# Kernel tuning notes

Measured on AMD Instinct MI355X. Metric: run time of the kernel, lower is better.

Reference implementation:

```python
import jax, jax.numpy as jnp
import numpy as np

B, L, H, C = 1, 512, 1024, 2


def setup_inputs() -> dict:
    key = jax.random.key(0)
    k1, k2, k3 = jax.random.split(key, 3)
    lm_output = jax.random.normal(k1, (B, L, H), dtype=jnp.float32)
    # torch Linear weight layout: [out_features, in_features]
    W1 = jax.random.normal(k2, (H, 2 * H), dtype=jnp.float32) * 0.02
    b1 = jnp.zeros((H,), dtype=jnp.float32)
    W2 = jax.random.normal(k3, (C, H), dtype=jnp.float32) * 0.02
    b2 = jnp.zeros((C,), dtype=jnp.float32)
    return {"lm_output": lm_output, "W1": W1, "b1": b1, "W2": W2, "b2": b2}


def reference(lm_output, W1, b1, W2, b2):
    # pair_emb[b,i,j] = concat(lm_output[b,j], lm_output[b,i])
    # Linear(concat(a,b)) decomposes: split W1 into the halves acting on each part.
    Wa = W1[:, :H]  # acts on lm_output_a (the j / column token)
    Wb = W1[:, H:]  # acts on lm_output_b (the i / row token)
    a_proj = jnp.einsum('blh,oh->blo', lm_output, Wa)  # [B,L,H]
    b_proj = jnp.einsum('blh,oh->blo', lm_output, Wb)  # [B,L,H]
    # hidden[b,i,j] = tanh(a_proj[b,j] + b_proj[b,i] + b1)   -> [B,L,L,H]
    hidden = jnp.tanh(a_proj[:, None, :, :] + b_proj[:, :, None, :] + b1)
    # Dropout is identity at inference time.
    logits = jnp.einsum('bijh,ch->bijc', hidden, W2) + b2  # [B,L,L,C]
    logits = (logits + jnp.swapaxes(logits, 1, 2)) / 2.0
    return logits
```

## Files before the change

kernel.cpp:

```cpp
#include <hip/hip_runtime.h>
#include <hip/hip_bf16.h>

#define HH 1024
#define LL 512
#define NT 16
#define NTRI 136

typedef __attribute__((ext_vector_type(8))) short bf16x8;
typedef __attribute__((ext_vector_type(4))) float f32x4;
typedef __attribute__((ext_vector_type(2))) float f32x2;

static constexpr float C_EXP = 2.8853900817779268f;

static __device__ __forceinline__ uint4 pack8(float4 a, float4 b) {
    union { uint4 u; __hip_bfloat162 h[4]; } r;
    r.h[0] = __float22bfloat162_rn(make_float2(a.x, a.y));
    r.h[1] = __float22bfloat162_rn(make_float2(a.z, a.w));
    r.h[2] = __float22bfloat162_rn(make_float2(b.x, b.y));
    r.h[3] = __float22bfloat162_rn(make_float2(b.z, b.w));
    return r.u;
}

__global__ __launch_bounds__(256, 4) void proj_mfma_kernel(
    const float* __restrict__ lm, const float* __restrict__ W1,
    const float* __restrict__ b1, float* __restrict__ Ea, float* __restrict__ Eb)
{
    __shared__ ushort As[64][136];
    __shared__ ushort Bs[64][136];

    const int tid  = threadIdx.x;
    const int lane = tid & 63;
    const int w    = tid >> 6;
    const int b    = blockIdx.x;
    const int xcd  = b & 7;
    const int idx  = b >> 3;
    const int nbase = (xcd * 4 + (idx & 3)) * 64;
    const int mbase = (idx >> 2) * 64;
    const int wm   = w * 16;
    const int sel  = nbase >> 10;
    const int nrow = nbase & 1023;

    const int frow = lane & 15;
    const int q8   = (lane >> 4) * 8;

    f32x4 acc[4] = {};

    for (int kb = 0; kb < HH; kb += 128) {
        __syncthreads();
        {
            int p = tid;
#pragma unroll
            for (int it = 0; it < 4; ++it, p += 256) {
                const int row = p >> 4, c8 = (p & 15) * 8;
                const float* pa = &lm[(mbase + row) * HH + kb + c8];
                *(uint4*)&As[row][c8] = pack8(*(const float4*)pa, *(const float4*)(pa + 4));
                const float* pw = &W1[(nrow + row) * 2048 + sel * 1024 + kb + c8];
                *(uint4*)&Bs[row][c8] = pack8(*(const float4*)pw, *(const float4*)(pw + 4));
            }
        }
        __syncthreads();

#pragma unroll
        for (int s = 0; s < 4; ++s) {
            const bf16x8 a = *(const bf16x8*)&As[wm + frow][s * 32 + q8];
#pragma unroll
            for (int nf = 0; nf < 4; ++nf) {
                const bf16x8 bb = *(const bf16x8*)&Bs[nf * 16 + frow][s * 32 + q8];
                acc[nf] = __builtin_amdgcn_mfma_f32_16x16x32_bf16(a, bb, acc[nf], 0, 0, 0);
            }
        }
    }

    const int col = lane & 15;
    const int rq  = (lane >> 4) * 4;
    const int m0  = mbase + wm + rq;
    const bool isA = sel == 0;
#pragma unroll
    for (int nf = 0; nf < 4; ++nf) {
        const int nn = (nrow + nf * 16 + col);
        if (isA) {
            const float bb = b1[nn];
#pragma unroll
            for (int r = 0; r < 4; ++r)
                Ea[(m0 + r) * HH + nn] = __builtin_amdgcn_exp2f(C_EXP * (acc[nf][r] + bb));
        } else {
#pragma unroll
            for (int r = 0; r < 4; ++r)
                Eb[(m0 + r) * HH + nn] = __builtin_amdgcn_exp2f(C_EXP * acc[nf][r]);
        }
    }
}

__global__ __launch_bounds__(256, 5) void pair_kernel(
    const float* __restrict__ Ea, const float* __restrict__ Eb,
    const float* __restrict__ W2, float* __restrict__ pbuf, int slice)
{
    __shared__ float tl[4][32][64];

    const int tid = threadIdx.x;
    const int tx  = tid & 15;
    const int ty  = tid >> 4;

    int tt = blockIdx.x, bi = 0, rem = NT;
    while (tt >= rem) { tt -= rem; --rem; ++bi; }
    const int bj    = bi + tt;
    const int ibase = bi * 32;
    const int jbase = bj * 32;
    const int k0    = blockIdx.y * slice;

    f32x2 aC0[2] = {}, aC1[2] = {};
    const f32x2 one2 = {1.f, 1.f};

    for (int kb = 0; kb < slice; kb += 64) {
        if (kb) __syncthreads();
        {
            int p = tid;
#pragma unroll
            for (int it = 0; it < 8; ++it, p += 256) {
                const int tile = p >> 9;
                const int row  = (p >> 4) & 31;
                const int c4   = p & 15;
                float4 v;
                if      (tile == 0) v = *(const float4*)&Ea[(jbase + row) * HH + k0 + kb + c4 * 4];
                else if (tile == 1) v = *(const float4*)&Ea[(ibase + row) * HH + k0 + kb + c4 * 4];
                else if (tile == 2) v = *(const float4*)&Eb[(ibase + row) * HH + k0 + kb + c4 * 4];
                else                v = *(const float4*)&Eb[(jbase + row) * HH + k0 + kb + c4 * 4];
                const int c4s = (tile == 0 || tile == 3) ? (c4 ^ (row & 15)) : c4;
                *(float4*)&tl[tile][row][c4s * 4] = v;
            }
        }
        __syncthreads();

#pragma unroll 4
        for (int h4 = 0; h4 < 16; ++h4) {
            const int sx = (h4 ^ tx) * 4;
            const float4 Aj0 = *(const float4*)&tl[0][tx][sx];
            const float4 Aj1 = *(const float4*)&tl[0][tx + 16][sx];
            const float4 Bj0 = *(const float4*)&tl[3][tx][sx];
            const float4 Bj1 = *(const float4*)&tl[3][tx + 16][sx];
            const float4 Ai0 = *(const float4*)&tl[1][ty][h4 * 4];
            const float4 Ai1 = *(const float4*)&tl[1][ty + 16][h4 * 4];
            const float4 Bi0 = *(const float4*)&tl[2][ty][h4 * 4];
            const float4 Bi1 = *(const float4*)&tl[2][ty + 16][h4 * 4];
            const float4 w0q = *(const float4*)&W2[k0 + kb + h4 * 4];
            const float4 w1q = *(const float4*)&W2[HH + k0 + kb + h4 * 4];

#define DO_H(AJ0v, AJ1v, BI0v, BI1v, AI0v, AI1v, BJ0v, BJ1v, W0s, W1s)        \
            {                                                                  \
                const f32x2 Aj = {AJ0v, AJ1v};                                 \
                const f32x2 Bj = {BJ0v, BJ1v};                                 \
                const f32x2 d0 = __builtin_elementwise_fma((f32x2){BI0v, BI0v}, Aj, one2); \
                const f32x2 d1 = __builtin_elementwise_fma((f32x2){BI1v, BI1v}, Aj, one2); \
                const f32x2 e0 = __builtin_elementwise_fma((f32x2){AI0v, AI0v}, Bj, one2); \
                const f32x2 e1 = __builtin_elementwise_fma((f32x2){AI1v, AI1v}, Bj, one2); \
                const float dp0 = d0.x * d0.y, dp1 = d1.x * d1.y;              \
                const float ep0 = e0.x * e0.y, ep1 = e1.x * e1.y;              \
                const float DR = __builtin_amdgcn_rcpf(dp0 * dp1);             \
                const float ER = __builtin_amdgcn_rcpf(ep0 * ep1);             \
                const f32x2 dq = (f32x2){DR, DR} * (f32x2){dp1, dp0};          \
                const f32x2 eq = (f32x2){ER, ER} * (f32x2){ep1, ep0};          \
                const f32x2 u0 = (f32x2){dq.x, dq.x} * d0.yx + (f32x2){eq.x, eq.x} * e0.yx; \
                const f32x2 u1 = (f32x2){dq.y, dq.y} * d1.yx + (f32x2){eq.y, eq.y} * e1.yx; \
                aC0[0] = __builtin_elementwise_fma(u0, (f32x2){(W0s), (W0s)}, aC0[0]); \
                aC1[0] = __builtin_elementwise_fma(u0, (f32x2){(W1s), (W1s)}, aC1[0]); \
                aC0[1] = __builtin_elementwise_fma(u1, (f32x2){(W0s), (W0s)}, aC0[1]); \
                aC1[1] = __builtin_elementwise_fma(u1, (f32x2){(W1s), (W1s)}, aC1[1]); \
            }
            DO_H(Aj0.x, Aj1.x, Bi0.x, Bi1.x, Ai0.x, Ai1.x, Bj0.x, Bj1.x, w0q.x, w1q.x)
            DO_H(Aj0.y, Aj1.y, Bi0.y, Bi1.y, Ai0.y, Ai1.y, Bj0.y, Bj1.y, w0q.y, w1q.y)
            DO_H(Aj0.z, Aj1.z, Bi0.z, Bi1.z, Ai0.z, Ai1.z, Bj0.z, Bj1.z, w0q.z, w1q.z)
            DO_H(Aj0.w, Aj1.w, Bi0.w, Bi1.w, Ai0.w, Ai1.w, Bj0.w, Bj1.w, w0q.w, w1q.w)
#undef DO_H
        }
    }

    float* pb = pbuf + ((size_t)blockIdx.y * NTRI + blockIdx.x) * 2048;
#pragma unroll
    for (int ii = 0; ii < 2; ++ii)
#pragma unroll
        for (int jj = 0; jj < 2; ++jj) {
            const int li = ty + ii * 16, lj = tx + jj * 16;
            const f32x2 v = { jj ? aC0[ii].y : aC0[ii].x,
                              jj ? aC1[ii].y : aC1[ii].x };
            *(f32x2*)&pb[(li * 32 + lj) * 2] = v;
        }
}

__global__ __launch_bounds__(256) void combine_kernel(
    const float* __restrict__ pbuf, const float* __restrict__ W2,
    const float* __restrict__ b2, float* __restrict__ out, int nz)
{
    __shared__ float s_ws[2];

    const int tid = threadIdx.x;
    if (tid < 128) {
        const int c = tid >> 6, l = tid & 63;
        float s = 0.f;
#pragma unroll
        for (int q = 0; q < 4; ++q) {
            const float4 v = *(const float4*)&W2[c * HH + (l + q * 64) * 4];
            s += v.x + v.y + v.z + v.w;
        }
#pragma unroll
        for (int off = 32; off; off >>= 1) s += __shfl_down(s, off, 64);
        if (l == 0) s_ws[c] = s + b2[c];
    }
    __syncthreads();

    const int idx   = blockIdx.x * 256 + tid;
    const int t     = idx >> 11;
    const int local = idx & 2047;
    int tt = t, bi = 0, rem = NT;
    while (tt >= rem) { tt -= rem; --rem; ++bi; }
    const int bj = bi + tt;

    float s0 = 0.f, s1 = 0.f;
    for (int z = 0; z < nz; z += 2) {
        s0 += pbuf[((size_t)z * NTRI + t) * 2048 + local];
        s1 += pbuf[((size_t)(z + 1) * NTRI + t) * 2048 + local];
    }
    const float s = s0 + s1;

    const int li = local >> 6;
    const int lj = (local >> 1) & 31;
    const int c  = local & 1;
    const float v = s_ws[c] - s;

    const int i = bi * 32 + li;
    const int j = bj * 32 + lj;
    out[(i * LL + j) * 2 + c] = v;
    out[(j * LL + i) * 2 + c] = v;
}

extern "C" void kernel_launch(void* const* d_in, const int* in_sizes, int n_in,
                              void* d_out, int out_size, void* d_ws, size_t ws_size,
                              hipStream_t stream)
{
    const float* lm = (const float*)d_in[0];
    const float* W1 = (const float*)d_in[1];
    const float* b1 = (const float*)d_in[2];
    const float* W2 = (const float*)d_in[3];
    const float* b2 = (const float*)d_in[4];
    float* out = (float*)d_out;

    char* ws = (char*)d_ws;
    float* Ea   = (float*)ws;
    float* Eb   = (float*)(ws + (2u << 20));
    float* pbuf = (float*)(ws + (4u << 20) + 64);

    const size_t ubase = (4u << 20) + 64;
    const size_t pb16  = (size_t)16 * NTRI * 2048 * 4;
    const int nz = (ws_size >= ubase + pb16) ? 16 : 8;
    const int slice = HH / nz;

    proj_mfma_kernel<<<256, 256, 0, stream>>>(lm, W1, b1, Ea, Eb);
    pair_kernel<<<dim3(NTRI, nz), 256, 0, stream>>>(Ea, Eb, W2, pbuf, slice);
    combine_kernel<<<(NTRI * 2048) / 256, 256, 0, stream>>>(pbuf, W2, b2, out, nz);
}
```

Measured before the change: 129.2 us.

## Prefetch pair tiles into registers, halve projection N-tile, fix split-K to 8

The pair kernel now loads the next 64-wide H chunk from global memory into registers while the current chunk is computed from LDS, a software double-buffer meant to hide global latency. The projection kernel uses 32-column N tiles with twice as many blocks so more CUs stay busy. Split-K is fixed at 8 slices instead of choosing 16 when workspace allows, which halves the partial buffer traffic but gives fewer pair blocks. The combine loop is unrolled by four. These changes cost extra registers in the pair kernel and less parallelism there.

```diff
diff --git a/kernel.cpp b/kernel.cpp
--- a/kernel.cpp
+++ b/kernel.cpp
@@ -5,6 +5,7 @@
 #define LL 512
 #define NT 16
 #define NTRI 136
+#define NZ 8
 
 typedef __attribute__((ext_vector_type(8))) short bf16x8;
 typedef __attribute__((ext_vector_type(4))) float f32x4;
@@ -26,7 +27,7 @@
     const float* __restrict__ b1, float* __restrict__ Ea, float* __restrict__ Eb)
 {
     __shared__ ushort As[64][136];
-    __shared__ ushort Bs[64][136];
+    __shared__ ushort Bs[32][136];
 
     const int tid  = threadIdx.x;
     const int lane = tid & 63;
@@ -34,8 +35,8 @@
     const int b    = blockIdx.x;
     const int xcd  = b & 7;
     const int idx  = b >> 3;
-    const int nbase = (xcd * 4 + (idx & 3)) * 64;
-    const int mbase = (idx >> 2) * 64;
+    const int nbase = (xcd * 8 + (idx & 7)) * 32;
+    const int mbase = (idx >> 3) * 64;
     const int wm   = w * 16;
     const int sel  = nbase >> 10;
     const int nrow = nbase & 1023;
@@ -43,7 +44,7 @@
     const int frow = lane & 15;
     const int q8   = (lane >> 4) * 8;
 
-    f32x4 acc[4] = {};
+    f32x4 acc[2] = {};
 
     for (int kb = 0; kb < HH; kb += 128) {
         __syncthreads();
@@ -54,6 +55,11 @@
                 const int row = p >> 4, c8 = (p & 15) * 8;
                 const float* pa = &lm[(mbase + row) * HH + kb + c8];
                 *(uint4*)&As[row][c8] = pack8(*(const float4*)pa, *(const float4*)(pa + 4));
+            }
+            int q = tid;
+#pragma unroll
+            for (int it = 0; it < 2; ++it, q += 256) {
+                const int row = q >> 4, c8 = (q & 15) * 8;
                 const float* pw = &W1[(nrow + row) * 2048 + sel * 1024 + kb + c8];
                 *(uint4*)&Bs[row][c8] = pack8(*(const float4*)pw, *(const float4*)(pw + 4));
             }
@@ -64,7 +70,7 @@
         for (int s = 0; s < 4; ++s) {
             const bf16x8 a = *(const bf16x8*)&As[wm + frow][s * 32 + q8];
 #pragma unroll
-            for (int nf = 0; nf < 4; ++nf) {
+            for (int nf = 0; nf < 2; ++nf) {
                 const bf16x8 bb = *(const bf16x8*)&Bs[nf * 16 + frow][s * 32 + q8];
                 acc[nf] = __builtin_amdgcn_mfma_f32_16x16x32_bf16(a, bb, acc[nf], 0, 0, 0);
             }
@@ -76,7 +82,7 @@
     const int m0  = mbase + wm + rq;
     const bool isA = sel == 0;
 #pragma unroll
-    for (int nf = 0; nf < 4; ++nf) {
+    for (int nf = 0; nf < 2; ++nf) {
         const int nn = (nrow + nf * 16 + col);
         if (isA) {
             const float bb = b1[nn];
@@ -111,68 +117,97 @@
     f32x2 aC0[2] = {}, aC1[2] = {};
     const f32x2 one2 = {1.f, 1.f};
 
+    float4 st[8];
+
+#define LOADS(hh)                                                              \
+    {                                                                          \
+        int p = tid;                                                           \
+        _Pragma("unroll")                                                      \
+        for (int it = 0; it < 8; ++it, p += 256) {                             \
+            const int tile = p >> 9;                                           \
+            const int row  = (p >> 4) & 31;                                    \
+            const int c4   = p & 15;                                           \
+            if      (tile == 0) st[it] = *(const float4*)&Ea[(jbase + row) * HH + (hh) + c4 * 4]; \
+            else if (tile == 1) st[it] = *(const float4*)&Ea[(ibase + row) * HH + (hh) + c4 * 4]; \
+            else if (tile == 2) st[it] = *(const float4*)&Eb[(ibase + row) * HH + (hh) + c4 * 4]; \
+            else                st[it] = *(const float4*)&Eb[(jbase + row) * HH + (hh) + c4 * 4]; \
+        }                                                                      \
+    }
+
+#define STORES()                                                               \
+    {                                                                          \
+        int p = tid;                                                           \
+        _Pragma("unroll")                                                      \
+        for (int it = 0; it < 8; ++it, p += 256) {                             \
+            const int tile = p >> 9;                                           \
+            const int row  = (p >> 4) & 31;                                    \
+            const int c4   = p & 15;                                           \
+            const int c4s  = (tile == 0 || tile == 3) ? (c4 ^ (row & 15)) : c4;\
+            *(float4*)&tl[tile][row][c4s * 4] = st[it];                        \
+        }                                                                      \
+    }
+
+#define COMPUTE(kb)                                                            \
+    _Pragma("unroll 4")                                                        \
+    for (int h4 = 0; h4 < 16; ++h4) {                                          \
+        const int sx = (h4 ^ tx) * 4;                 \
+        const float4 Aj0 = *(const float4*)&tl[0][tx][sx];                     \
+        const float4 Aj1 = *(const float4*)&tl[0][tx + 16][sx];                \
+        const float4 Bj0 = *(const float4*)&tl[3][tx][sx];                     \
+        const float4 Bj1 = *(const float4*)&tl[3][tx + 16][sx];                \
+        const float4 Ai0 = *(const float4*)&tl[1][ty][h4 * 4];                 \
+        const float4 Ai1 = *(const float4*)&tl[1][ty + 16][h4 * 4];            \
+        const float4 Bi0 = *(const float4*)&tl[2][ty][h4 * 4];                 \
+        const float4 Bi1 = *(const float4*)&tl[2][ty + 16][h4 * 4];            \
+        const float4 w0q = *(const float4*)&W2[k0 + (kb) + h4 * 4];            \
+        const float4 w1q = *(const float4*)&W2[HH + k0 + (kb) + h4 * 4];       \
+        DO_H(Aj0.x, Aj1.x, Bi0.x, Bi1.x, Ai0.x, Ai1.x, Bj0.x, Bj1.x, w0q.x, w1q.x) \
+        DO_H(Aj0.y, Aj1.y, Bi0.y, Bi1.y, Ai0.y, Ai1.y, Bj0.y, Bj1.y, w0q.y, w1q.y) \
+        DO_H(Aj0.z, Aj1.z, Bi0.z, Bi1.z, Ai0.z, Ai1.z, Bj0.z, Bj1.z, w0q.z, w1q.z) \
+        DO_H(Aj0.w, Aj1.w, Bi0.w, Bi1.w, Ai0.w, Ai1.w, Bj0.w, Bj1.w, w0q.w, w1q.w) \
+    }
+
+#define DO_H(AJ0v, AJ1v, BI0v, BI1v, AI0v, AI1v, BJ0v, BJ1v, W0s, W1s)        \
+    {                                                                          \
+        const f32x2 Aj = {AJ0v, AJ1v};                                         \
+        const f32x2 Bj = {BJ0v, BJ1v};                                         \
+        const f32x2 d0 = __builtin_elementwise_fma((f32x2){BI0v, BI0v}, Aj, one2); \
+        const f32x2 d1 = __builtin_elementwise_fma((f32x2){BI1v, BI1v}, Aj, one2); \
+        const f32x2 e0 = __builtin_elementwise_fma((f32x2){AI0v, AI0v}, Bj, one2); \
+        const f32x2 e1 = __builtin_elementwise_fma((f32x2){AI1v, AI1v}, Bj, one2); \
+        const float dp0 = d0.x * d0.y, dp1 = d1.x * d1.y;                      \
+        const float ep0 = e0.x * e0.y, ep1 = e1.x * e1.y;                      \
+        const float DR = __builtin_amdgcn_rcpf(dp0 * dp1);                     \
+        const float ER = __builtin_amdgcn_rcpf(ep0 * ep1);                     \
+        const f32x2 dq = (f32x2){DR, DR} * (f32x2){dp1, dp0};                  \
+        const f32x2 eq = (f32x2){ER, ER} * (f32x2){ep1, ep0};                  \
+        const f32x2 u0 = (f32x2){dq.x, dq.x} * __builtin_shufflevector(d0, d0, 1, 0) \
+                       + (f32x2){eq.x, eq.x} * __builtin_shufflevector(e0, e0, 1, 0); \
+        const f32x2 u1 = (f32x2){dq.y, dq.y} * __builtin_shufflevector(d1, d1, 1, 0) \
+                       + (f32x2){eq.y, eq.y} * __builtin_shufflevector(e1, e1, 1, 0); \
+        aC0[0] = __builtin_elementwise_fma(u0, (f32x2){(W0s), (W0s)}, aC0[0]); \
+        aC1[0] = __builtin_elementwise_fma(u0, (f32x2){(W1s), (W1s)}, aC1[0]); \
+        aC0[1] = __builtin_elementwise_fma(u1, (f32x2){(W0s), (W0s)}, aC0[1]); \
+        aC1[1] = __builtin_elementwise_fma(u1, (f32x2){(W1s), (W1s)}, aC1[1]); \
+    }
+
+    LOADS(k0);
+    STORES();
     for (int kb = 0; kb < slice; kb += 64) {
-        if (kb) __syncthreads();
-        {
-            int p = tid;
-#pragma unroll
-            for (int it = 0; it < 8; ++it, p += 256) {
-                const int tile = p >> 9;
-                const int row  = (p >> 4) & 31;
-                const int c4   = p & 15;
-                float4 v;
-                if      (tile == 0) v = *(const float4*)&Ea[(jbase + row) * HH + k0 + kb + c4 * 4];
-                else if (tile == 1) v = *(const float4*)&Ea[(ibase + row) * HH + k0 + kb + c4 * 4];
-                else if (tile == 2) v = *(const float4*)&Eb[(ibase + row) * HH + k0 + kb + c4 * 4];
-                else                v = *(const float4*)&Eb[(jbase + row) * HH + k0 + kb + c4 * 4];
-                const int c4s = (tile == 0 || tile == 3) ? (c4 ^ (row & 15)) : c4;
-                *(float4*)&tl[tile][row][c4s * 4] = v;
-            }
-        }
+        const bool more = (kb + 64 < slice);
+        if (more) LOADS(k0 + kb + 64);
         __syncthreads();
-
-#pragma unroll 4
-        for (int h4 = 0; h4 < 16; ++h4) {
-            const int sx = (h4 ^ tx) * 4;
-            const float4 Aj0 = *(const float4*)&tl[0][tx][sx];
-            const float4 Aj1 = *(const float4*)&tl[0][tx + 16][sx];
-            const float4 Bj0 = *(const float4*)&tl[3][tx][sx];
-            const float4 Bj1 = *(const float4*)&tl[3][tx + 16][sx];
-            const float4 Ai0 = *(const float4*)&tl[1][ty][h4 * 4];
-            const float4 Ai1 = *(const float4*)&tl[1][ty + 16][h4 * 4];
-            const float4 Bi0 = *(const float4*)&tl[2][ty][h4 * 4];
-            const float4 Bi1 = *(const float4*)&tl[2][ty + 16][h4 * 4];
-            const float4 w0q = *(const float4*)&W2[k0 + kb + h4 * 4];
-            const float4 w1q = *(const float4*)&W2[HH + k0 + kb + h4 * 4];
-
-#define DO_H(AJ0v, AJ1v, BI0v, BI1v, AI0v, AI1v, BJ0v, BJ1v, W0s, W1s)        \
-            {                                                                  \
-                const f32x2 Aj = {AJ0v, AJ1v};                                 \
-                const f32x2 Bj = {BJ0v, BJ1v};                                 \
-                const f32x2 d0 = __builtin_elementwise_fma((f32x2){BI0v, BI0v}, Aj, one2); \
-                const f32x2 d1 = __builtin_elementwise_fma((f32x2){BI1v, BI1v}, Aj, one2); \
-                const f32x2 e0 = __builtin_elementwise_fma((f32x2){AI0v, AI0v}, Bj, one2); \
-                const f32x2 e1 = __builtin_elementwise_fma((f32x2){AI1v, AI1v}, Bj, one2); \
-                const float dp0 = d0.x * d0.y, dp1 = d1.x * d1.y;              \
-                const float ep0 = e0.x * e0.y, ep1 = e1.x * e1.y;              \
-                const float DR = __builtin_amdgcn_rcpf(dp0 * dp1);             \
-                const float ER = __builtin_amdgcn_rcpf(ep0 * ep1);             \
-                const f32x2 dq = (f32x2){DR, DR} * (f32x2){dp1, dp0};          \
-                const f32x2 eq = (f32x2){ER, ER} * (f32x2){ep1, ep0};          \
-                const f32x2 u0 = (f32x2){dq.x, dq.x} * d0.yx + (f32x2){eq.x, eq.x} * e0.yx; \
-                const f32x2 u1 = (f32x2){dq.y, dq.y} * d1.yx + (f32x2){eq.y, eq.y} * e1.yx; \
-                aC0[0] = __builtin_elementwise_fma(u0, (f32x2){(W0s), (W0s)}, aC0[0]); \
-                aC1[0] = __builtin_elementwise_fma(u0, (f32x2){(W1s), (W1s)}, aC1[0]); \
-                aC0[1] = __builtin_elementwise_fma(u1, (f32x2){(W0s), (W0s)}, aC0[1]); \
-                aC1[1] = __builtin_elementwise_fma(u1, (f32x2){(W1s), (W1s)}, aC1[1]); \
-            }
-            DO_H(Aj0.x, Aj1.x, Bi0.x, Bi1.x, Ai0.x, Ai1.x, Bj0.x, Bj1.x, w0q.x, w1q.x)
-            DO_H(Aj0.y, Aj1.y, Bi0.y, Bi1.y, Ai0.y, Ai1.y, Bj0.y, Bj1.y, w0q.y, w1q.y)
-            DO_H(Aj0.z, Aj1.z, Bi0.z, Bi1.z, Ai0.z, Ai1.z, Bj0.z, Bj1.z, w0q.z, w1q.z)
-            DO_H(Aj0.w, Aj1.w, Bi0.w, Bi1.w, Ai0.w, Ai1.w, Bj0.w, Bj1.w, w0q.w, w1q.w)
+        COMPUTE(kb)
+        if (more) {
+            __syncthreads();
+            STORES();
+        }
+    }
+
 #undef DO_H
-        }
-    }
+#undef COMPUTE
+#undef STORES
+#undef LOADS
 
     float* pb = pbuf + ((size_t)blockIdx.y * NTRI + blockIdx.x) * 2048;
 #pragma unroll
@@ -214,12 +249,14 @@
     while (tt >= rem) { tt -= rem; --rem; ++bi; }
     const int bj = bi + tt;
 
-    float s0 = 0.f, s1 = 0.f;
-    for (int z = 0; z < nz; z += 2) {
+    float s0 = 0.f, s1 = 0.f, s2 = 0.f, s3 = 0.f;
+    for (int z = 0; z < nz; z += 4) {
         s0 += pbuf[((size_t)z * NTRI + t) * 2048 + local];
         s1 += pbuf[((size_t)(z + 1) * NTRI + t) * 2048 + local];
-    }
-    const float s = s0 + s1;
+        s2 += pbuf[((size_t)(z + 2) * NTRI + t) * 2048 + local];
+        s3 += pbuf[((size_t)(z + 3) * NTRI + t) * 2048 + local];
+    }
+    const float s = (s0 + s1) + (s2 + s3);
 
     const int li = local >> 6;
     const int lj = (local >> 1) & 31;
@@ -248,12 +285,10 @@
     float* Eb   = (float*)(ws + (2u << 20));
     float* pbuf = (float*)(ws + (4u << 20) + 64);
 
-    const size_t ubase = (4u << 20) + 64;
-    const size_t pb16  = (size_t)16 * NTRI * 2048 * 4;
-    const int nz = (ws_size >= ubase + pb16) ? 16 : 8;
+    const int nz = NZ;
     const int slice = HH / nz;
 
-    proj_mfma_kernel<<<256, 256, 0, stream>>>(lm, W1, b1, Ea, Eb);
+    proj_mfma_kernel<<<512, 256, 0, stream>>>(lm, W1, b1, Ea, Eb);
     pair_kernel<<<dim3(NTRI, nz), 256, 0, stream>>>(Ea, Eb, W2, pbuf, slice);
     combine_kernel<<<(NTRI * 2048) / 256, 256, 0, stream>>>(pbuf, W2, b2, out, nz);
 }
```

New measurement: 139.1 us. 7.6% more time.
